# Kernel tuning notes

Measured on AMD Instinct MI355X. Metric: run time of the kernel, lower is better.

## Reference

```python
import jax, jax.numpy as jnp
import numpy as np

EPS = 1e-5
NHEAD = 8

def layer_norm(x, g, b):
    mu = jnp.mean(x, axis=-1, keepdims=True)
    var = jnp.mean((x - mu) ** 2, axis=-1, keepdims=True)
    return (x - mu) * jax.lax.rsqrt(var + EPS) * g + b

def setup_inputs() -> dict:
    key = jax.random.key(0)
    ks = jax.random.split(key, 8)
    B, S, D, F = 4, 2048, 512, 2048
    s = 0.02
    return {
        "x": jax.random.normal(ks[0], (B, S, D), jnp.float32),
        "Wqkv": jax.random.normal(ks[1], (3 * D, D), jnp.float32) * s,
        "bqkv": jnp.zeros((3 * D,), jnp.float32),
        "Wo": jax.random.normal(ks[2], (D, D), jnp.float32) * s,
        "bo": jnp.zeros((D,), jnp.float32),
        "W1": jax.random.normal(ks[3], (F, D), jnp.float32) * s,
        "b1": jnp.zeros((F,), jnp.float32),
        "W2": jax.random.normal(ks[4], (D, F), jnp.float32) * s,
        "b2": jnp.zeros((D,), jnp.float32),
        "g1": jnp.ones((D,), jnp.float32),
        "bn1": jnp.zeros((D,), jnp.float32),
        "g2": jnp.ones((D,), jnp.float32),
        "bn2": jnp.zeros((D,), jnp.float32),
    }

def reference(x, Wqkv, bqkv, Wo, bo, W1, b1, W2, b2, g1, bn1, g2, bn2):
    B, S, D = x.shape
    H = NHEAD
    hd = D // H
    # fused QKV projection (torch MultiheadAttention in_proj)
    qkv = x @ Wqkv.T + bqkv                      # [B,S,3D]
    q, k, v = jnp.split(qkv, 3, axis=-1)
    q = q.reshape(B, S, H, hd).transpose(0, 2, 1, 3)  # [B,H,S,hd]
    k = k.reshape(B, S, H, hd).transpose(0, 2, 1, 3)
    v = v.reshape(B, S, H, hd).transpose(0, 2, 1, 3)
    scores = jnp.einsum("bhqd,bhkd->bhqk", q, k) / jnp.sqrt(jnp.float32(hd))
    causal = jnp.tril(jnp.ones((S, S), bool))
    scores = jnp.where(causal, scores, jnp.float32(-jnp.inf))
    attn = jax.nn.softmax(scores, axis=-1)
    ctx = jnp.einsum("bhqk,bhkd->bhqd", attn, v)        # [B,H,S,hd]
    ctx = ctx.transpose(0, 2, 1, 3).reshape(B, S, D)
    attn_out = ctx @ Wo.T + bo
    # residual + LayerNorm 1
    x = layer_norm(x + attn_out, g1, bn1)
    # FFN (ReLU) + residual + LayerNorm 2
    ff = jax.nn.relu(x @ W1.T + b1) @ W2.T + b2
    x = layer_norm(x + ff, g2, bn2)
    return x
```

## Files before the change

kernel.cpp:

```cpp
#include <hip/hip_runtime.h>
#include <hip/hip_bf16.h>
#include <math.h>

#define D_MODEL 512
#define SEQ     2048
#define BATCH   4
#define NHEADS  8
#define HDIM    64
#define FFN     2048
#define TOKENS  (BATCH*SEQ)

typedef __attribute__((ext_vector_type(8))) short bf16x8;
typedef __attribute__((ext_vector_type(4))) float f32x4;
typedef __attribute__((ext_vector_type(4))) unsigned u32x4;

__device__ inline ushort f2bf(float f) {
    unsigned u = __builtin_bit_cast(unsigned, f);
    unsigned r = (u + 0x7fffu + ((u >> 16) & 1u)) >> 16;
    return (ushort)r;
}

#define GLOAD_LDS16(g, l) __builtin_amdgcn_global_load_lds( \
    (const __attribute__((address_space(1))) void*)(g), \
    (__attribute__((address_space(3))) void*)(l), 16, 0, 0)

__global__ void cast_all_bf16(const float* __restrict__ x, const float* __restrict__ Wqkv,
                              const float* __restrict__ Wo, const float* __restrict__ W1,
                              const float* __restrict__ W2, ushort* __restrict__ outbase) {
    const int i = blockIdx.x * blockDim.x + threadIdx.x;
    if (i >= 1835008) return;
    float4 v;
    if      (i < 1048576) v = ((const float4*)x)[i];
    else if (i < 1245184) v = ((const float4*)Wqkv)[i - 1048576];
    else if (i < 1310720) v = ((const float4*)Wo)[i - 1245184];
    else if (i < 1572864) v = ((const float4*)W1)[i - 1310720];
    else                  v = ((const float4*)W2)[i - 1572864];
    ushort4 o;
    o.x = f2bf(v.x); o.y = f2bf(v.y); o.z = f2bf(v.z); o.w = f2bf(v.w);
    ((ushort4*)outbase)[i] = o;
}

template<int MODE, int RELU>
__global__ __launch_bounds__(256) void gemm_bt_mfma(const ushort* __restrict__ A,
                                                    const ushort* __restrict__ W,
                                                    const float* __restrict__ bias,
                                                    void* __restrict__ CoutA,
                                                    void* __restrict__ CoutB,
                                                    ushort* __restrict__ Qc,
                                                    ushort* __restrict__ Kc,
                                                    ushort* __restrict__ Vt,
                                                    int M, int N, int Kstride, int Klen) {
    __shared__ ushort Asb[3][128 * 32];
    __shared__ ushort Bsb[3][128 * 32];

    const int tid  = threadIdx.x;
    const int lane = tid & 63;
    const int wv   = tid >> 6;

    const int Gx = gridDim.x;
    const int f  = blockIdx.x + Gx * blockIdx.y;
    const int xc = f & 7;
    const int j  = f >> 3;
    const int ni = j % Gx;
    const int mi = xc * 8 + j / Gx;
    const int m0 = mi * 128;
    const int n0 = ni * 128;

    const int wm   = (wv >> 1) * 64;
    const int wn   = (wv & 1) * 64;
    const int ksel = (MODE == 3) ? blockIdx.z : 0;

    const ushort* Ab = A + (size_t)ksel * Klen;
    const ushort* Wb = W + (size_t)ksel * Klen;

    const int rA = wv * 32 + (lane >> 2);
    const int cS = (((lane & 3) ^ ((lane >> 3) & 3)) * 8);
    const ushort* gA0 = Ab + (size_t)(m0 + rA) * Kstride + cS;
    const ushort* gA1 = gA0 + (size_t)16 * Kstride;
    const ushort* gB0 = Wb + (size_t)(n0 + rA) * Kstride + cS;
    const ushort* gB1 = gB0 + (size_t)16 * Kstride;

    f32x4 acc[4][4] = {};

    const int fr  = lane & 15;
    const int fks = (((lane >> 4) ^ ((fr >> 1) & 3)) * 8);
    const int lo  = wv * 1024;

#define STAGE(ab, bb) do { \
        GLOAD_LDS16(gA0, (ab) + lo); \
        GLOAD_LDS16(gA1, (ab) + lo + 512); \
        GLOAD_LDS16(gB0, (bb) + lo); \
        GLOAD_LDS16(gB1, (bb) + lo + 512); \
        gA0 += 32; gA1 += 32; gB0 += 32; gB1 += 32; } while (0)

#define COMPUTE(ab, bb) do { \
        bf16x8 af_[4], bf_[4]; \
        _Pragma("unroll") \
        for (int i_ = 0; i_ < 4; ++i_) \
            af_[i_] = *(const bf16x8*)((ab) + (wm + i_ * 16 + fr) * 32 + fks); \
        _Pragma("unroll") \
        for (int j_ = 0; j_ < 4; ++j_) \
            bf_[j_] = *(const bf16x8*)((bb) + (wn + j_ * 16 + fr) * 32 + fks); \
        _Pragma("unroll") \
        for (int i_ = 0; i_ < 4; ++i_) \
            _Pragma("unroll") \
            for (int j_ = 0; j_ < 4; ++j_) \
                acc[i_][j_] = __builtin_amdgcn_mfma_f32_16x16x32_bf16(af_[i_], bf_[j_], acc[i_][j_], 0, 0, 0); \
        } while (0)

    ushort *Ac = Asb[0], *An = Asb[1], *As = Asb[2];
    ushort *Bc = Bsb[0], *Bn = Bsb[1], *Bs = Bsb[2];

    STAGE(Ac, Bc);
    STAGE(An, Bn);
    const int ntiles = Klen >> 5;
    for (int t = 0; t < ntiles - 1; ++t) {
        asm volatile("s_waitcnt vmcnt(4)" ::: "memory");
        __builtin_amdgcn_s_barrier();
        __builtin_amdgcn_sched_barrier(0);
        if (t + 2 < ntiles) STAGE(As, Bs);
        COMPUTE(Ac, Bc);
        ushort* tA = Ac; Ac = An; An = As; As = tA;
        ushort* tB = Bc; Bc = Bn; Bn = Bs; Bs = tB;
    }
    asm volatile("s_waitcnt vmcnt(0)" ::: "memory");
    __builtin_amdgcn_s_barrier();
    __builtin_amdgcn_sched_barrier(0);
    COMPUTE(Ac, Bc);

#undef STAGE
#undef COMPUTE

    const int col  = lane & 15;
    const int rowq = (lane >> 4) * 4;
    #pragma unroll
    for (int i = 0; i < 4; ++i) {
        const int gm = m0 + wm + i * 16 + rowq;
        #pragma unroll
        for (int j2 = 0; j2 < 4; ++j2) {
            const int gn = n0 + wn + j2 * 16 + col;
            if (MODE == 2) {
                const float bv = bias[gn];
                const int seg = gn >> 9;
                const int h   = (gn >> 6) & 7;
                const int dd  = gn & 63;
                const int bb  = gm >> 11;
                const int ss  = gm & 2047;
                const int bh  = bb * 8 + h;
                if (seg == 2) {
                    ushort4 pk;
                    pk.x = f2bf(acc[i][j2][0] + bv);
                    pk.y = f2bf(acc[i][j2][1] + bv);
                    pk.z = f2bf(acc[i][j2][2] + bv);
                    pk.w = f2bf(acc[i][j2][3] + bv);
                    *(ushort4*)(Vt + ((size_t)bh * 64 + dd) * 2048 + ss) = pk;
                } else {
                    ushort* dst = (seg == 0 ? Qc : Kc) + ((size_t)bh * 2048 + ss) * 64 + dd;
                    #pragma unroll
                    for (int r = 0; r < 4; ++r)
                        dst[(size_t)r * 64] = f2bf(acc[i][j2][r] + bv);
                }
            } else if (MODE == 3) {
                float* dst = (float*)(ksel ? CoutB : CoutA);
                const float bv = ksel ? 0.f : bias[gn];
                #pragma unroll
                for (int r = 0; r < 4; ++r)
                    dst[(size_t)(gm + r) * N + gn] = acc[i][j2][r] + bv;
            } else {
                const float bv = bias[gn];
                #pragma unroll
                for (int r = 0; r < 4; ++r) {
                    float v = acc[i][j2][r] + bv;
                    if (RELU) v = fmaxf(v, 0.f);
                    ((ushort*)CoutA)[(size_t)(gm + r) * N + gn] = f2bf(v);
                }
            }
        }
    }
}

__device__ __forceinline__ void attn_step(const ushort* __restrict__ Kb,
                                          const ushort* __restrict__ Vb,
                                          bf16x8 qf0, bf16x8 qf1,
                                          float& lp, f32x4 (&o)[4],
                                          int qw, int j0, bool diag,
                                          int col, int g, int c7) {
    f32x4 s[4] = {};
    #pragma unroll
    for (int nt = 0; nt < 4; ++nt) {
        const int kr = nt * 16 + col;
        bf16x8 kf0 = *(const bf16x8*)(Kb + kr * 64 + (((g    ) ^ c7) * 8));
        bf16x8 kf1 = *(const bf16x8*)(Kb + kr * 64 + (((g + 4) ^ c7) * 8));
        s[nt] = __builtin_amdgcn_mfma_f32_16x16x32_bf16(kf0, qf0, s[nt], 0, 0, 0);
        s[nt] = __builtin_amdgcn_mfma_f32_16x16x32_bf16(kf1, qf1, s[nt], 0, 0, 0);
    }

    if (diag) {
        #pragma unroll
        for (int nt = 0; nt < 4; ++nt)
            #pragma unroll
            for (int r = 0; r < 4; ++r)
                if ((j0 + nt * 16 + 4 * g + r) > (qw + col)) s[nt][r] = -INFINITY;
    }

    unsigned W[8];
    #pragma unroll
    for (int nt = 0; nt < 4; ++nt) {
        float p0 = __expf(s[nt][0] * 0.125f);
        float p1 = __expf(s[nt][1] * 0.125f);
        float p2 = __expf(s[nt][2] * 0.125f);
        float p3 = __expf(s[nt][3] * 0.125f);
        lp += (p0 + p1) + (p2 + p3);
        asm("v_cvt_pk_bf16_f32 %0, %1, %2" : "=v"(W[2 * nt])     : "v"(p0), "v"(p1));
        asm("v_cvt_pk_bf16_f32 %0, %1, %2" : "=v"(W[2 * nt + 1]) : "v"(p2), "v"(p3));
    }
    asm("v_permlane32_swap_b32 %0, %1" : "+v"(W[0]), "+v"(W[2]));
    asm("v_permlane32_swap_b32 %0, %1" : "+v"(W[1]), "+v"(W[3]));
    asm("v_permlane32_swap_b32 %0, %1" : "+v"(W[4]), "+v"(W[6]));
    asm("v_permlane32_swap_b32 %0, %1" : "+v"(W[5]), "+v"(W[7]));
    asm("v_permlane16_swap_b32 %0, %1" : "+v"(W[0]), "+v"(W[2]));
    asm("v_permlane16_swap_b32 %0, %1" : "+v"(W[1]), "+v"(W[3]));
    asm("v_permlane16_swap_b32 %0, %1" : "+v"(W[4]), "+v"(W[6]));
    asm("v_permlane16_swap_b32 %0, %1" : "+v"(W[5]), "+v"(W[7]));

    u32x4 wa = {W[0], W[1], W[2], W[3]};
    u32x4 wb = {W[4], W[5], W[6], W[7]};
    bf16x8 pf0 = __builtin_bit_cast(bf16x8, wa);
    bf16x8 pf1 = __builtin_bit_cast(bf16x8, wb);

    #pragma unroll
    for (int nt = 0; nt < 4; ++nt) {
        const int vr = nt * 16 + col;
        bf16x8 vf0 = *(const bf16x8*)(Vb + vr * 64 + (((g    ) ^ c7) * 8));
        bf16x8 vf1 = *(const bf16x8*)(Vb + vr * 64 + (((g + 4) ^ c7) * 8));
        o[nt] = __builtin_amdgcn_mfma_f32_16x16x32_bf16(pf0, vf0, o[nt], 0, 0, 0);
        o[nt] = __builtin_amdgcn_mfma_f32_16x16x32_bf16(pf1, vf1, o[nt], 0, 0, 0);
    }
}

__global__ __launch_bounds__(256, 4) void attn_mfma_kernel(const ushort* __restrict__ Qc,
                                                           const ushort* __restrict__ Kc,
                                                           const ushort* __restrict__ Vt,
                                                           ushort* __restrict__ ctxb) {
    __shared__ ushort Ks[2 * 64 * 64];
    __shared__ ushort Vs[2 * 64 * 64];

    const int tid  = threadIdx.x;
    const int lane = tid & 63;
    const int wv   = tid >> 6;
    const int idx  = blockIdx.x;
    const int bh   = (idx & 7) * 4 + (idx >> 7);
    const int pair = (idx >> 3) & 15;
    const int q0a  = pair * 64;
    const int q0b  = (31 - pair) * 64;
    const int qwA  = q0a + wv * 16;
    const int qwB  = q0b + wv * 16;

    const int col = lane & 15;
    const int g   = lane >> 4;
    const int c7  = col & 7;

    bf16x8 qfA0, qfA1, qfB0, qfB1;
    {
        const ushort* qa = Qc + ((size_t)bh * 2048 + qwA + col) * 64 + g * 8;
        qfA0 = *(const bf16x8*)qa;
        qfA1 = *(const bf16x8*)(qa + 32);
        const ushort* qb = Qc + ((size_t)bh * 2048 + qwB + col) * 64 + g * 8;
        qfB0 = *(const bf16x8*)qb;
        qfB1 = *(const bf16x8*)(qb + 32);
    }

    const int srow = tid >> 2;
    const int sch  = 2 * (tid & 3);
    const ushort* Kg = Kc + ((size_t)bh * 2048 + srow) * 64 + sch * 8;
    const ushort* Vg = Vt + ((size_t)bh * 64 + srow) * 2048 + sch * 8;
    const int ko0 = srow * 64 + (((sch    ) ^ (srow & 7)) * 8);
    const int ko1 = srow * 64 + (((sch + 1) ^ (srow & 7)) * 8);

    float lpa = 0.f, lpb = 0.f;
    f32x4 oa[4] = {}, ob[4] = {};

    bf16x8 pk0 = *(const bf16x8*)(Kg);
    bf16x8 pk1 = *(const bf16x8*)(Kg + 8);
    bf16x8 pv0 = *(const bf16x8*)(Vg);
    bf16x8 pv1 = *(const bf16x8*)(Vg + 8);

    for (int j0 = 0; j0 <= q0b; j0 += 64) {
        const int par = (j0 >> 6) & 1;
        ushort* Kb = Ks + par * 4096;
        ushort* Vb = Vs + par * 4096;
        *(bf16x8*)(Kb + ko0) = pk0; *(bf16x8*)(Kb + ko1) = pk1;
        *(bf16x8*)(Vb + ko0) = pv0; *(bf16x8*)(Vb + ko1) = pv1;
        __syncthreads();

        if (j0 < q0b) {
            pk0 = *(const bf16x8*)(Kg + (size_t)(j0 + 64) * 64);
            pk1 = *(const bf16x8*)(Kg + (size_t)(j0 + 64) * 64 + 8);
            pv0 = *(const bf16x8*)(Vg + j0 + 64);
            pv1 = *(const bf16x8*)(Vg + j0 + 72);
        }

        if (j0 <= q0a)
            attn_step(Kb, Vb, qfA0, qfA1, lpa, oa, qwA, j0, j0 == q0a, col, g, c7);
        attn_step(Kb, Vb, qfB0, qfB1, lpb, ob, qwB, j0, j0 == q0b, col, g, c7);
    }

    float la = lpa; la += __shfl_xor(la, 16); la += __shfl_xor(la, 32);
    float lb = lpb; lb += __shfl_xor(lb, 16); lb += __shfl_xor(lb, 32);
    const int b = bh >> 3, h = bh & 7;
    #pragma unroll
    for (int r = 0; r < 4; ++r) {
        const float inva = 1.f / __shfl(la, 4 * g + r);
        const float invb = 1.f / __shfl(lb, 4 * g + r);
        const size_t rowa = ((size_t)b * 2048 + qwA + 4 * g + r) * 512 + h * 64;
        const size_t rowb = ((size_t)b * 2048 + qwB + 4 * g + r) * 512 + h * 64;
        #pragma unroll
        for (int nt = 0; nt < 4; ++nt) {
            ctxb[rowa + nt * 16 + col] = f2bf(oa[nt][r] * inva);
            ctxb[rowb + nt * 16 + col] = f2bf(ob[nt][r] * invb);
        }
    }
}

template<int WRITE_BF16>
__global__ void ln_residual(const float* __restrict__ A, const float* __restrict__ B1,
                            const float* __restrict__ B2,
                            const float* __restrict__ g, const float* __restrict__ beta,
                            float* __restrict__ out, ushort* __restrict__ outb) {
    __shared__ float sbuf[8];
    const int row = blockIdx.x;
    const int tid = threadIdx.x;
    const size_t base = (size_t)row * D_MODEL;

    float v0 = A[base + tid]       + B1[base + tid]       + B2[base + tid];
    float v1 = A[base + tid + 256] + B1[base + tid + 256] + B2[base + tid + 256];

    float sum = v0 + v1;
    #pragma unroll
    for (int off = 32; off; off >>= 1) sum += __shfl_xor(sum, off);
    if ((tid & 63) == 0) sbuf[tid >> 6] = sum;
    __syncthreads();
    if (tid == 0) { float t = 0.f; for (int i = 0; i < 4; ++i) t += sbuf[i]; sbuf[4] = t; }
    __syncthreads();
    const float mu = sbuf[4] * (1.f / 512.f);
    __syncthreads();

    float d0 = v0 - mu, d1 = v1 - mu;
    float sq = d0 * d0 + d1 * d1;
    #pragma unroll
    for (int off = 32; off; off >>= 1) sq += __shfl_xor(sq, off);
    if ((tid & 63) == 0) sbuf[tid >> 6] = sq;
    __syncthreads();
    if (tid == 0) { float t = 0.f; for (int i = 0; i < 4; ++i) t += sbuf[i]; sbuf[4] = t; }
    __syncthreads();
    const float var = sbuf[4] * (1.f / 512.f);
    const float rs  = rsqrtf(var + 1e-5f);

    float r0 = d0 * rs * g[tid]       + beta[tid];
    float r1 = d1 * rs * g[tid + 256] + beta[tid + 256];
    out[base + tid]       = r0;
    out[base + tid + 256] = r1;
    if (WRITE_BF16) {
        outb[base + tid]       = f2bf(r0);
        outb[base + tid + 256] = f2bf(r1);
    }
}

extern "C" void kernel_launch(void* const* d_in, const int* in_sizes, int n_in,
                              void* d_out, int out_size, void* d_ws, size_t ws_size,
                              hipStream_t stream) {
    const float* x    = (const float*)d_in[0];
    const float* Wqkv = (const float*)d_in[1];
    const float* bqkv = (const float*)d_in[2];
    const float* Wo   = (const float*)d_in[3];
    const float* bo   = (const float*)d_in[4];
    const float* W1   = (const float*)d_in[5];
    const float* b1   = (const float*)d_in[6];
    const float* W2   = (const float*)d_in[7];
    const float* b2   = (const float*)d_in[8];
    const float* g1   = (const float*)d_in[9];
    const float* bn1  = (const float*)d_in[10];
    const float* g2   = (const float*)d_in[11];
    const float* bn2  = (const float*)d_in[12];

    float* ws = (float*)d_ws;
    ushort* Qcb     = (ushort*)ws;
    ushort* Kcb     = (ushort*)(ws + 2097152);
    ushort* Vtb     = (ushort*)(ws + 4194304);
    float*  attn_b  = ws;
    ushort* ff1b    = (ushort*)ws;
    float*  ff2a    = ws + 8388608;
    float*  attn_a  = ws + 12582912;
    float*  ff2b    = ws + 12582912;
    float*  ln1     = ws + 16777216;
    ushort* ctxb  = (ushort*)(ws + 20971520);
    ushort* ln1b  = (ushort*)(ws + 23068672);
    ushort* xb    = (ushort*)(ws + 25165824);
    ushort* Wqkvb = (ushort*)(ws + 27262976);
    float*  out   = (float*)d_out;
    ushort* W1b   = (ushort*)(ws + 27787264);
    ushort* W2b   = (ushort*)(ws + 28311552);
    ushort* Wob   = (ushort*)(ws + 27656192);

    const dim3 blk(256);

    cast_all_bf16<<<dim3(7168), blk, 0, stream>>>(x, Wqkv, Wo, W1, W2, xb);

    gemm_bt_mfma<2,0><<<dim3(1536/128, 8192/128), blk, 0, stream>>>(
        xb, Wqkvb, bqkv, nullptr, nullptr, Qcb, Kcb, Vtb, TOKENS, 1536, 512, 512);
    attn_mfma_kernel<<<dim3(512), blk, 0, stream>>>(Qcb, Kcb, Vtb, ctxb);
    gemm_bt_mfma<3,0><<<dim3(512/128, 8192/128, 2), blk, 0, stream>>>(
        ctxb, Wob, bo, attn_a, attn_b, nullptr, nullptr, nullptr, TOKENS, 512, 512, 256);
    ln_residual<1><<<dim3(TOKENS), blk, 0, stream>>>(x, attn_a, attn_b, g1, bn1, ln1, ln1b);
    gemm_bt_mfma<1,1><<<dim3(2048/128, 8192/128), blk, 0, stream>>>(
        ln1b, W1b, b1, ff1b, nullptr, nullptr, nullptr, nullptr, TOKENS, 2048, 512, 512);
    gemm_bt_mfma<3,0><<<dim3(512/128, 8192/128, 2), blk, 0, stream>>>(
        ff1b, W2b, b2, ff2a, ff2b, nullptr, nullptr, nullptr, TOKENS, 512, 2048, 1024);
    ln_residual<0><<<dim3(TOKENS), blk, 0, stream>>>(ln1, ff2a, ff2b, g2, bn2, out, nullptr);
}
```

Before: 248.9 us.

## Split paired attention tiles into one tile per block, longest first; add MFMA priority hints

The attention kernel no longer has each block handle a mirrored pair of query tiles (short and long) sharing K/V loads. It launches twice as many blocks, each owning one 64-row query tile, ordered so the longest causal tiles are scheduled first for better load balance. It also wraps MFMA sequences in the GEMM and attention inner loops with s_setprio raises so matrix work gets issue priority. The cost is that K/V tiles are now loaded separately per query tile instead of shared across the pair, roughly doubling attention K/V traffic.

Measured after the change: 251.9 us. About the same (+1.2%).

```diff
diff --git a/kernel.cpp b/kernel.cpp
--- a/kernel.cpp
+++ b/kernel.cpp
@@ -101,11 +101,13 @@
         _Pragma("unroll") \
         for (int j_ = 0; j_ < 4; ++j_) \
             bf_[j_] = *(const bf16x8*)((bb) + (wn + j_ * 16 + fr) * 32 + fks); \
+        __builtin_amdgcn_s_setprio(1); \
         _Pragma("unroll") \
         for (int i_ = 0; i_ < 4; ++i_) \
             _Pragma("unroll") \
             for (int j_ = 0; j_ < 4; ++j_) \
                 acc[i_][j_] = __builtin_amdgcn_mfma_f32_16x16x32_bf16(af_[i_], bf_[j_], acc[i_][j_], 0, 0, 0); \
+        __builtin_amdgcn_s_setprio(0); \
         } while (0)
 
     ushort *Ac = Asb[0], *An = Asb[1], *As = Asb[2];
@@ -186,6 +188,7 @@
                                           int qw, int j0, bool diag,
                                           int col, int g, int c7) {
     f32x4 s[4] = {};
+    __builtin_amdgcn_s_setprio(1);
     #pragma unroll
     for (int nt = 0; nt < 4; ++nt) {
         const int kr = nt * 16 + col;
@@ -194,6 +197,7 @@
         s[nt] = __builtin_amdgcn_mfma_f32_16x16x32_bf16(kf0, qf0, s[nt], 0, 0, 0);
         s[nt] = __builtin_amdgcn_mfma_f32_16x16x32_bf16(kf1, qf1, s[nt], 0, 0, 0);
     }
+    __builtin_amdgcn_s_setprio(0);
 
     if (diag) {
         #pragma unroll
@@ -228,6 +232,7 @@
     bf16x8 pf0 = __builtin_bit_cast(bf16x8, wa);
     bf16x8 pf1 = __builtin_bit_cast(bf16x8, wb);
 
+    __builtin_amdgcn_s_setprio(1);
     #pragma unroll
     for (int nt = 0; nt < 4; ++nt) {
         const int vr = nt * 16 + col;
@@ -236,6 +241,7 @@
         o[nt] = __builtin_amdgcn_mfma_f32_16x16x32_bf16(pf0, vf0, o[nt], 0, 0, 0);
         o[nt] = __builtin_amdgcn_mfma_f32_16x16x32_bf16(pf1, vf1, o[nt], 0, 0, 0);
     }
+    __builtin_amdgcn_s_setprio(0);
 }
 
 __global__ __launch_bounds__(256, 4) void attn_mfma_kernel(const ushort* __restrict__ Qc,
@@ -249,25 +255,21 @@
     const int lane = tid & 63;
     const int wv   = tid >> 6;
     const int idx  = blockIdx.x;
-    const int bh   = (idx & 7) * 4 + (idx >> 7);
-    const int pair = (idx >> 3) & 15;
-    const int q0a  = pair * 64;
-    const int q0b  = (31 - pair) * 64;
-    const int qwA  = q0a + wv * 16;
-    const int qwB  = q0b + wv * 16;
+    const int slot = idx >> 3;
+    const int bh   = (idx & 7) * 4 + (slot & 3);
+    const int qt   = 31 - (slot >> 2);
+    const int q0   = qt * 64;
+    const int qw   = q0 + wv * 16;
 
     const int col = lane & 15;
     const int g   = lane >> 4;
     const int c7  = col & 7;
 
-    bf16x8 qfA0, qfA1, qfB0, qfB1;
+    bf16x8 qf0, qf1;
     {
-        const ushort* qa = Qc + ((size_t)bh * 2048 + qwA + col) * 64 + g * 8;
-        qfA0 = *(const bf16x8*)qa;
-        qfA1 = *(const bf16x8*)(qa + 32);
-        const ushort* qb = Qc + ((size_t)bh * 2048 + qwB + col) * 64 + g * 8;
-        qfB0 = *(const bf16x8*)qb;
-        qfB1 = *(const bf16x8*)(qb + 32);
+        const ushort* qa = Qc + ((size_t)bh * 2048 + qw + col) * 64 + g * 8;
+        qf0 = *(const bf16x8*)qa;
+        qf1 = *(const bf16x8*)(qa + 32);
     }
 
     const int srow = tid >> 2;
@@ -277,15 +279,15 @@
     const int ko0 = srow * 64 + (((sch    ) ^ (srow & 7)) * 8);
     const int ko1 = srow * 64 + (((sch + 1) ^ (srow & 7)) * 8);
 
-    float lpa = 0.f, lpb = 0.f;
-    f32x4 oa[4] = {}, ob[4] = {};
+    float lp = 0.f;
+    f32x4 o[4] = {};
 
     bf16x8 pk0 = *(const bf16x8*)(Kg);
     bf16x8 pk1 = *(const bf16x8*)(Kg + 8);
     bf16x8 pv0 = *(const bf16x8*)(Vg);
     bf16x8 pv1 = *(const bf16x8*)(Vg + 8);
 
-    for (int j0 = 0; j0 <= q0b; j0 += 64) {
+    for (int j0 = 0; j0 <= q0; j0 += 64) {
         const int par = (j0 >> 6) & 1;
         ushort* Kb = Ks + par * 4096;
         ushort* Vb = Vs + par * 4096;
@@ -293,32 +295,25 @@
         *(bf16x8*)(Vb + ko0) = pv0; *(bf16x8*)(Vb + ko1) = pv1;
         __syncthreads();
 
-        if (j0 < q0b) {
+        if (j0 < q0) {
             pk0 = *(const bf16x8*)(Kg + (size_t)(j0 + 64) * 64);
             pk1 = *(const bf16x8*)(Kg + (size_t)(j0 + 64) * 64 + 8);
             pv0 = *(const bf16x8*)(Vg + j0 + 64);
             pv1 = *(const bf16x8*)(Vg + j0 + 72);
         }
 
-        if (j0 <= q0a)
-            attn_step(Kb, Vb, qfA0, qfA1, lpa, oa, qwA, j0, j0 == q0a, col, g, c7);
-        attn_step(Kb, Vb, qfB0, qfB1, lpb, ob, qwB, j0, j0 == q0b, col, g, c7);
-    }
-
-    float la = lpa; la += __shfl_xor(la, 16); la += __shfl_xor(la, 32);
-    float lb = lpb; lb += __shfl_xor(lb, 16); lb += __shfl_xor(lb, 32);
+        attn_step(Kb, Vb, qf0, qf1, lp, o, qw, j0, j0 == q0, col, g, c7);
+    }
+
+    float la = lp; la += __shfl_xor(la, 16); la += __shfl_xor(la, 32);
     const int b = bh >> 3, h = bh & 7;
     #pragma unroll
     for (int r = 0; r < 4; ++r) {
         const float inva = 1.f / __shfl(la, 4 * g + r);
-        const float invb = 1.f / __shfl(lb, 4 * g + r);
-        const size_t rowa = ((size_t)b * 2048 + qwA + 4 * g + r) * 512 + h * 64;
-        const size_t rowb = ((size_t)b * 2048 + qwB + 4 * g + r) * 512 + h * 64;
+        const size_t rowa = ((size_t)b * 2048 + qw + 4 * g + r) * 512 + h * 64;
         #pragma unroll
-        for (int nt = 0; nt < 4; ++nt) {
-            ctxb[rowa + nt * 16 + col] = f2bf(oa[nt][r] * inva);
-            ctxb[rowb + nt * 16 + col] = f2bf(ob[nt][r] * invb);
-        }
+        for (int nt = 0; nt < 4; ++nt)
+            ctxb[rowa + nt * 16 + col] = f2bf(o[nt][r] * inva);
     }
 }
 
@@ -408,7 +403,7 @@
 
     gemm_bt_mfma<2,0><<<dim3(1536/128, 8192/128), blk, 0, stream>>>(
         xb, Wqkvb, bqkv, nullptr, nullptr, Qcb, Kcb, Vtb, TOKENS, 1536, 512, 512);
-    attn_mfma_kernel<<<dim3(512), blk, 0, stream>>>(Qcb, Kcb, Vtb, ctxb);
+    attn_mfma_kernel<<<dim3(1024), blk, 0, stream>>>(Qcb, Kcb, Vtb, ctxb);
     gemm_bt_mfma<3,0><<<dim3(512/128, 8192/128, 2), blk, 0, stream>>>(
         ctxb, Wob, bo, attn_a, attn_b, nullptr, nullptr, nullptr, TOKENS, 512, 512, 256);
     ln_residual<1><<<dim3(TOKENS), blk, 0, stream>>>(x, attn_a, attn_b, g1, bn1, ln1, ln1b);
```

## Replace split-K N=512 GEMMs with 64-row tiles and prioritize attention MFMAs

Applied to the files above, without the earlier changes.

The two N=512 GEMMs (out-proj and FFN2) no longer use split-K with two partial fp32 outputs. Each now uses a full-K pass over a 64-row M tile, which keeps the block count the same while removing one partial-sum write and read in the layernorm kernels. The GEMM is templated on BM, with matching LDS staging and wait counts. Attention MFMA sections are also wrapped in s_setprio to raise wave priority during matrix work. The trade-off is less A-tile reuse per block and longer K loops for the 64-row tiles.

New measurement: 246.7 us. About the same (-0.9%).

```diff
diff --git a/kernel.cpp b/kernel.cpp
--- a/kernel.cpp
+++ b/kernel.cpp
@@ -40,17 +40,17 @@
     ((ushort4*)outbase)[i] = o;
 }
 
-template<int MODE, int RELU>
+template<int MODE, int RELU, int BM>
 __global__ __launch_bounds__(256) void gemm_bt_mfma(const ushort* __restrict__ A,
                                                     const ushort* __restrict__ W,
                                                     const float* __restrict__ bias,
                                                     void* __restrict__ CoutA,
-                                                    void* __restrict__ CoutB,
                                                     ushort* __restrict__ Qc,
                                                     ushort* __restrict__ Kc,
                                                     ushort* __restrict__ Vt,
                                                     int M, int N, int Kstride, int Klen) {
-    __shared__ ushort Asb[3][128 * 32];
+    constexpr int MI = BM / 32;
+    __shared__ ushort Asb[3][BM * 32];
     __shared__ ushort Bsb[3][128 * 32];
 
     const int tid  = threadIdx.x;
@@ -62,52 +62,57 @@
     const int xc = f & 7;
     const int j  = f >> 3;
     const int ni = j % Gx;
-    const int mi = xc * 8 + j / Gx;
-    const int m0 = mi * 128;
+    const int mi = xc * (gridDim.y >> 3) + j / Gx;
+    const int m0 = mi * BM;
     const int n0 = ni * 128;
 
-    const int wm   = (wv >> 1) * 64;
-    const int wn   = (wv & 1) * 64;
-    const int ksel = (MODE == 3) ? blockIdx.z : 0;
-
-    const ushort* Ab = A + (size_t)ksel * Klen;
-    const ushort* Wb = W + (size_t)ksel * Klen;
-
-    const int rA = wv * 32 + (lane >> 2);
+    const int wm = (wv >> 1) * (BM / 2);
+    const int wn = (wv & 1) * 64;
+
+    const int rA = wv * (BM / 4) + (lane >> 2);
+    const int rB = wv * 32 + (lane >> 2);
     const int cS = (((lane & 3) ^ ((lane >> 3) & 3)) * 8);
-    const ushort* gA0 = Ab + (size_t)(m0 + rA) * Kstride + cS;
+    const ushort* gA0 = A + (size_t)(m0 + rA) * Kstride + cS;
     const ushort* gA1 = gA0 + (size_t)16 * Kstride;
-    const ushort* gB0 = Wb + (size_t)(n0 + rA) * Kstride + cS;
+    const ushort* gB0 = W + (size_t)(n0 + rB) * Kstride + cS;
     const ushort* gB1 = gB0 + (size_t)16 * Kstride;
 
-    f32x4 acc[4][4] = {};
+    f32x4 acc[MI][4] = {};
 
     const int fr  = lane & 15;
     const int fks = (((lane >> 4) ^ ((fr >> 1) & 3)) * 8);
-    const int lo  = wv * 1024;
+    const int loA = wv * (BM * 32 / 4);
+    const int loB = wv * 1024;
 
 #define STAGE(ab, bb) do { \
-        GLOAD_LDS16(gA0, (ab) + lo); \
-        GLOAD_LDS16(gA1, (ab) + lo + 512); \
-        GLOAD_LDS16(gB0, (bb) + lo); \
-        GLOAD_LDS16(gB1, (bb) + lo + 512); \
-        gA0 += 32; gA1 += 32; gB0 += 32; gB1 += 32; } while (0)
+        GLOAD_LDS16(gA0, (ab) + loA); \
+        if constexpr (BM == 128) GLOAD_LDS16(gA1, (ab) + loA + 512); \
+        GLOAD_LDS16(gB0, (bb) + loB); \
+        GLOAD_LDS16(gB1, (bb) + loB + 512); \
+        gA0 += 32; if constexpr (BM == 128) gA1 += 32; \
+        gB0 += 32; gB1 += 32; } while (0)
 
 #define COMPUTE(ab, bb) do { \
-        bf16x8 af_[4], bf_[4]; \
+        bf16x8 af_[MI], bf_[4]; \
         _Pragma("unroll") \
-        for (int i_ = 0; i_ < 4; ++i_) \
+        for (int i_ = 0; i_ < MI; ++i_) \
             af_[i_] = *(const bf16x8*)((ab) + (wm + i_ * 16 + fr) * 32 + fks); \
         _Pragma("unroll") \
         for (int j_ = 0; j_ < 4; ++j_) \
             bf_[j_] = *(const bf16x8*)((bb) + (wn + j_ * 16 + fr) * 32 + fks); \
         _Pragma("unroll") \
-        for (int i_ = 0; i_ < 4; ++i_) \
+        for (int i_ = 0; i_ < MI; ++i_) \
             _Pragma("unroll") \
             for (int j_ = 0; j_ < 4; ++j_) \
                 acc[i_][j_] = __builtin_amdgcn_mfma_f32_16x16x32_bf16(af_[i_], bf_[j_], acc[i_][j_], 0, 0, 0); \
         } while (0)
 
+#define PWAIT do { \
+        if constexpr (BM == 128) asm volatile("s_waitcnt vmcnt(4)" ::: "memory"); \
+        else                     asm volatile("s_waitcnt vmcnt(3)" ::: "memory"); \
+        __builtin_amdgcn_s_barrier(); \
+        __builtin_amdgcn_sched_barrier(0); } while (0)
+
     ushort *Ac = Asb[0], *An = Asb[1], *As = Asb[2];
     ushort *Bc = Bsb[0], *Bn = Bsb[1], *Bs = Bsb[2];
 
@@ -115,9 +120,7 @@
     STAGE(An, Bn);
     const int ntiles = Klen >> 5;
     for (int t = 0; t < ntiles - 1; ++t) {
-        asm volatile("s_waitcnt vmcnt(4)" ::: "memory");
-        __builtin_amdgcn_s_barrier();
-        __builtin_amdgcn_sched_barrier(0);
+        PWAIT;
         if (t + 2 < ntiles) STAGE(As, Bs);
         COMPUTE(Ac, Bc);
         ushort* tA = Ac; Ac = An; An = As; As = tA;
@@ -130,11 +133,12 @@
 
 #undef STAGE
 #undef COMPUTE
+#undef PWAIT
 
     const int col  = lane & 15;
     const int rowq = (lane >> 4) * 4;
     #pragma unroll
-    for (int i = 0; i < 4; ++i) {
+    for (int i = 0; i < MI; ++i) {
         const int gm = m0 + wm + i * 16 + rowq;
         #pragma unroll
         for (int j2 = 0; j2 < 4; ++j2) {
@@ -161,8 +165,8 @@
                         dst[(size_t)r * 64] = f2bf(acc[i][j2][r] + bv);
                 }
             } else if (MODE == 3) {
-                float* dst = (float*)(ksel ? CoutB : CoutA);
-                const float bv = ksel ? 0.f : bias[gn];
+                float* dst = (float*)CoutA;
+                const float bv = bias[gn];
                 #pragma unroll
                 for (int r = 0; r < 4; ++r)
                     dst[(size_t)(gm + r) * N + gn] = acc[i][j2][r] + bv;
@@ -186,6 +190,7 @@
                                           int qw, int j0, bool diag,
                                           int col, int g, int c7) {
     f32x4 s[4] = {};
+    __builtin_amdgcn_s_setprio(1);
     #pragma unroll
     for (int nt = 0; nt < 4; ++nt) {
         const int kr = nt * 16 + col;
@@ -194,6 +199,7 @@
         s[nt] = __builtin_amdgcn_mfma_f32_16x16x32_bf16(kf0, qf0, s[nt], 0, 0, 0);
         s[nt] = __builtin_amdgcn_mfma_f32_16x16x32_bf16(kf1, qf1, s[nt], 0, 0, 0);
     }
+    __builtin_amdgcn_s_setprio(0);
 
     if (diag) {
         #pragma unroll
@@ -228,6 +234,7 @@
     bf16x8 pf0 = __builtin_bit_cast(bf16x8, wa);
     bf16x8 pf1 = __builtin_bit_cast(bf16x8, wb);
 
+    __builtin_amdgcn_s_setprio(1);
     #pragma unroll
     for (int nt = 0; nt < 4; ++nt) {
         const int vr = nt * 16 + col;
@@ -236,6 +243,7 @@
         o[nt] = __builtin_amdgcn_mfma_f32_16x16x32_bf16(pf0, vf0, o[nt], 0, 0, 0);
         o[nt] = __builtin_amdgcn_mfma_f32_16x16x32_bf16(pf1, vf1, o[nt], 0, 0, 0);
     }
+    __builtin_amdgcn_s_setprio(0);
 }
 
 __global__ __launch_bounds__(256, 4) void attn_mfma_kernel(const ushort* __restrict__ Qc,
@@ -324,7 +332,6 @@
 
 template<int WRITE_BF16>
 __global__ void ln_residual(const float* __restrict__ A, const float* __restrict__ B1,
-                            const float* __restrict__ B2,
                             const float* __restrict__ g, const float* __restrict__ beta,
                             float* __restrict__ out, ushort* __restrict__ outb) {
     __shared__ float sbuf[8];
@@ -332,8 +339,8 @@
     const int tid = threadIdx.x;
     const size_t base = (size_t)row * D_MODEL;
 
-    float v0 = A[base + tid]       + B1[base + tid]       + B2[base + tid];
-    float v1 = A[base + tid + 256] + B1[base + tid + 256] + B2[base + tid + 256];
+    float v0 = A[base + tid]       + B1[base + tid];
+    float v1 = A[base + tid + 256] + B1[base + tid + 256];
 
     float sum = v0 + v1;
     #pragma unroll
@@ -387,11 +394,9 @@
     ushort* Qcb     = (ushort*)ws;
     ushort* Kcb     = (ushort*)(ws + 2097152);
     ushort* Vtb     = (ushort*)(ws + 4194304);
-    float*  attn_b  = ws;
     ushort* ff1b    = (ushort*)ws;
     float*  ff2a    = ws + 8388608;
     float*  attn_a  = ws + 12582912;
-    float*  ff2b    = ws + 12582912;
     float*  ln1     = ws + 16777216;
     ushort* ctxb  = (ushort*)(ws + 20971520);
     ushort* ln1b  = (ushort*)(ws + 23068672);
@@ -406,15 +411,15 @@
 
     cast_all_bf16<<<dim3(7168), blk, 0, stream>>>(x, Wqkv, Wo, W1, W2, xb);
 
-    gemm_bt_mfma<2,0><<<dim3(1536/128, 8192/128), blk, 0, stream>>>(
-        xb, Wqkvb, bqkv, nullptr, nullptr, Qcb, Kcb, Vtb, TOKENS, 1536, 512, 512);
+    gemm_bt_mfma<2,0,128><<<dim3(1536/128, 8192/128), blk, 0, stream>>>(
+        xb, Wqkvb, bqkv, nullptr, Qcb, Kcb, Vtb, TOKENS, 1536, 512, 512);
     attn_mfma_kernel<<<dim3(512), blk, 0, stream>>>(Qcb, Kcb, Vtb, ctxb);
-    gemm_bt_mfma<3,0><<<dim3(512/128, 8192/128, 2), blk, 0, stream>>>(
-        ctxb, Wob, bo, attn_a, attn_b, nullptr, nullptr, nullptr, TOKENS, 512, 512, 256);
-    ln_residual<1><<<dim3(TOKENS), blk, 0, stream>>>(x, attn_a, attn_b, g1, bn1, ln1, ln1b);
-    gemm_bt_mfma<1,1><<<dim3(2048/128, 8192/128), blk, 0, stream>>>(
-        ln1b, W1b, b1, ff1b, nullptr, nullptr, nullptr, nullptr, TOKENS, 2048, 512, 512);
-    gemm_bt_mfma<3,0><<<dim3(512/128, 8192/128, 2), blk, 0, stream>>>(
-        ff1b, W2b, b2, ff2a, ff2b, nullptr, nullptr, nullptr, TOKENS, 512, 2048, 1024);
-    ln_residual<0><<<dim3(TOKENS), blk, 0, stream>>>(ln1, ff2a, ff2b, g2, bn2, out, nullptr);
-}
+    gemm_bt_mfma<3,0,64><<<dim3(512/128, 8192/64), blk, 0, stream>>>(
+        ctxb, Wob, bo, attn_a, nullptr, nullptr, nullptr, TOKENS, 512, 512, 512);
+    ln_residual<1><<<dim3(TOKENS), blk, 0, stream>>>(x, attn_a, g1, bn1, ln1, ln1b);
+    gemm_bt_mfma<1,1,128><<<dim3(2048/128, 8192/128), blk, 0, stream>>>(
+        ln1b, W1b, b1, ff1b, nullptr, nullptr, nullptr, TOKENS, 2048, 512, 512);
+    gemm_bt_mfma<3,0,64><<<dim3(512/128, 8192/64), blk, 0, stream>>>(
+        ff1b, W2b, b2, ff2a, nullptr, nullptr, nullptr, TOKENS, 512, 2048, 2048);
+    ln_residual<0><<<dim3(TOKENS), blk, 0, stream>>>(ln1, ff2a, g2, bn2, out, nullptr);
+}
```
